# Optimization experiments

Hardware: AMD Instinct MI355X
Metric: run time of the kernel (lower is better)

## Reference

```python
import jax, jax.numpy as jnp
import numpy as np

TH = 0.8  # ratio-test threshold (init kwarg)


def _cdist(d1, d2):
    # Euclidean distance matrix: ||a||^2 + ||b||^2 - 2 a.b, clamped and sqrt'd
    d1_sq = jnp.sum(d1 * d1, axis=1, keepdims=True)          # [B1,1]
    d2_sq = jnp.sum(d2 * d2, axis=1, keepdims=True).T        # [1,B2]
    dm = d1_sq + d2_sq - 2.0 * (d1 @ d2.T)                   # [B1,B2]
    return jnp.sqrt(jnp.clip(dm, 0.0, None))


def setup_inputs() -> dict:
    key = jax.random.key(0)
    k1, k2 = jax.random.split(key)
    desc1 = jax.random.normal(k1, (8192, 512), dtype=jnp.float32)
    desc2 = jax.random.normal(k2, (8192, 512), dtype=jnp.float32)
    return {"desc1": desc1, "desc2": desc2}


def reference(desc1, desc2):
    # match_snn: nearest + second-nearest neighbor, Lowe ratio test.
    # jit-friendly padded form: instead of compacting rows passing the ratio
    # test (data-dependent B3), we return full-size (B1,) arrays plus the
    # boolean validity mask; masked entries have dist 0.
    dm = _cdist(desc1, desc2)                                # [B1,B2]
    neg_vals, idxs = jax.lax.top_k(-dm, 2)                   # two smallest
    vals = -neg_vals                                         # [B1,2]
    ratio = vals[:, 0] / vals[:, 1]                          # [B1]
    mask = ratio <= TH                                       # [B1]
    match_dists = jnp.where(mask, ratio, 0.0).reshape(-1, 1)  # [B1,1]
    idxs_in1 = jnp.arange(desc1.shape[0], dtype=jnp.int32)
    matches_idxs = jnp.stack([idxs_in1, idxs[:, 0]], axis=1)  # [B1,2]
    return match_dists, matches_idxs, mask
```

## Files before the change

kernel.cpp:

```cpp
#include <hip/hip_runtime.h>

#define NROWS 8192
#define DIM   512

typedef __attribute__((ext_vector_type(8))) short short8;
typedef __attribute__((ext_vector_type(4))) float f32x4;

__device__ inline unsigned short f2bf(float x) {
    unsigned u = __float_as_uint(x);
    u += 0x7fffu + ((u >> 16) & 1u);
    return (unsigned short)(u >> 16);
}
__device__ inline float bf2f(unsigned short h) {
    return __uint_as_float(((unsigned)h) << 16);
}

__global__ __launch_bounds__(256) void dm_split(const float* __restrict__ d1,
                                                const float* __restrict__ d2,
                                                unsigned short* __restrict__ Ahi,
                                                unsigned short* __restrict__ Alo,
                                                unsigned short* __restrict__ Bhi,
                                                unsigned short* __restrict__ Blo) {
    const long long t = (long long)blockIdx.x * 256 + threadIdx.x;
    const long long e = t * 8;
    const long long half = (long long)NROWS * DIM;
    const bool second = (e >= half);
    const float* src = second ? d2 : d1;
    unsigned short* hid = second ? Bhi : Ahi;
    unsigned short* lod = second ? Blo : Alo;
    const long long o = second ? e - half : e;
    float4 x0 = *(const float4*)(src + o);
    float4 x1 = *(const float4*)(src + o + 4);
    float xs[8] = {x0.x, x0.y, x0.z, x0.w, x1.x, x1.y, x1.z, x1.w};
    unsigned short hs[8], ls[8];
#pragma unroll
    for (int i = 0; i < 8; ++i) {
        hs[i] = f2bf(xs[i]);
        ls[i] = f2bf(xs[i] - bf2f(hs[i]));
    }
    *(short8*)(hid + o) = *(short8*)hs;
    *(short8*)(lod + o) = *(short8*)ls;
}

__global__ __launch_bounds__(256) void dm_norms2(const float* __restrict__ d2,
                                                 float* __restrict__ n2) {
    const int wave = threadIdx.x >> 6;
    const int lane = threadIdx.x & 63;
    const int r = blockIdx.x * 4 + wave;
    const float* src = d2 + (size_t)r * DIM;
    float4 a = *(const float4*)(src + lane * 4);
    float4 b = *(const float4*)(src + 256 + lane * 4);
    float s = a.x * a.x + a.y * a.y + a.z * a.z + a.w * a.w
            + b.x * b.x + b.y * b.y + b.z * b.z + b.w * b.w;
#pragma unroll
    for (int m = 32; m >= 1; m >>= 1) s += __shfl_xor(s, m);
    if (lane == 0) n2[r] = s;
}

#define NSPLIT 16
#define SLICE (NROWS / NSPLIT)
#define NCT   (SLICE / 128)
#define NKT   48

__global__ __launch_bounds__(256, 2) void dm_match_mfma(
        const unsigned short* __restrict__ Ahi, const unsigned short* __restrict__ Alo,
        const unsigned short* __restrict__ Bhi, const unsigned short* __restrict__ Blo,
        const float* __restrict__ n2, float4* __restrict__ part) {
    __shared__ short8 Bs[8][64];

    const int tid = threadIdx.x;
    const int l   = tid & 63;
    const int w   = tid >> 6;
    const int rb  = blockIdx.x >> 4;
    const int sp  = blockIdx.x & (NSPLIT - 1);
    const int row0 = rb * 128;
    const int col0 = sp * SLICE;
    const int lr = l & 15;
    const int lk = l >> 4;

    const long long arow0 = (long long)(row0 + (2 * w + 0) * 16 + lr) * DIM + lk * 8;
    const long long arow1 = (long long)(row0 + (2 * w + 1) * 16 + lr) * DIM + lk * 8;

    float v0[8], v1[8];
    int   i0[8], i1[8];
#pragma unroll
    for (int s = 0; s < 8; ++s) { v0[s] = 3.0e38f; v1[s] = 3.0e38f; i0[s] = 0; i1[s] = 0; }

    for (int ct = 0; ct < NCT; ++ct) {
        const int colblk = col0 + ct * 128;
        const long long brow0 = (long long)(colblk + (2 * w + 0) * 16 + lr) * DIM + lk * 8;
        const long long brow1 = (long long)(colblk + (2 * w + 1) * 16 + lr) * DIM + lk * 8;

        f32x4 acc[2][8];
#pragma unroll
        for (int m = 0; m < 2; ++m)
#pragma unroll
            for (int n = 0; n < 8; ++n) acc[m][n] = (f32x4){0.f, 0.f, 0.f, 0.f};

        short8 ga0 = *(const short8*)(Ahi + arow0);
        short8 ga1 = *(const short8*)(Ahi + arow1);
        short8 gb0 = *(const short8*)(Bhi + brow0);
        short8 gb1 = *(const short8*)(Bhi + brow1);

        for (int kt = 0; kt < NKT; ++kt) {
            const int kn = (kt + 1 < NKT) ? kt + 1 : kt;
            const int pn = kn >> 4;
            const unsigned short* An = (pn < 2) ? Ahi : Alo;
            const unsigned short* Bn = (pn == 1) ? Blo : Bhi;
            const int k0n = (kn & 15) * 32;
            short8 na0 = *(const short8*)(An + arow0 + k0n);
            short8 na1 = *(const short8*)(An + arow1 + k0n);
            short8 nb0 = *(const short8*)(Bn + brow0 + k0n);
            short8 nb1 = *(const short8*)(Bn + brow1 + k0n);

            __syncthreads();
            Bs[2 * w + 0][l] = gb0;
            Bs[2 * w + 1][l] = gb1;
            __syncthreads();

            short8 b0 = Bs[0][l], b1 = Bs[1][l], b2 = Bs[2][l], b3 = Bs[3][l];
            short8 b4 = Bs[4][l], b5 = Bs[5][l], b6 = Bs[6][l], b7 = Bs[7][l];

            acc[0][0] = __builtin_amdgcn_mfma_f32_16x16x32_bf16(ga0, b0, acc[0][0], 0, 0, 0);
            acc[0][1] = __builtin_amdgcn_mfma_f32_16x16x32_bf16(ga0, b1, acc[0][1], 0, 0, 0);
            acc[0][2] = __builtin_amdgcn_mfma_f32_16x16x32_bf16(ga0, b2, acc[0][2], 0, 0, 0);
            acc[0][3] = __builtin_amdgcn_mfma_f32_16x16x32_bf16(ga0, b3, acc[0][3], 0, 0, 0);
            acc[0][4] = __builtin_amdgcn_mfma_f32_16x16x32_bf16(ga0, b4, acc[0][4], 0, 0, 0);
            acc[0][5] = __builtin_amdgcn_mfma_f32_16x16x32_bf16(ga0, b5, acc[0][5], 0, 0, 0);
            acc[0][6] = __builtin_amdgcn_mfma_f32_16x16x32_bf16(ga0, b6, acc[0][6], 0, 0, 0);
            acc[0][7] = __builtin_amdgcn_mfma_f32_16x16x32_bf16(ga0, b7, acc[0][7], 0, 0, 0);
            acc[1][0] = __builtin_amdgcn_mfma_f32_16x16x32_bf16(ga1, b0, acc[1][0], 0, 0, 0);
            acc[1][1] = __builtin_amdgcn_mfma_f32_16x16x32_bf16(ga1, b1, acc[1][1], 0, 0, 0);
            acc[1][2] = __builtin_amdgcn_mfma_f32_16x16x32_bf16(ga1, b2, acc[1][2], 0, 0, 0);
            acc[1][3] = __builtin_amdgcn_mfma_f32_16x16x32_bf16(ga1, b3, acc[1][3], 0, 0, 0);
            acc[1][4] = __builtin_amdgcn_mfma_f32_16x16x32_bf16(ga1, b4, acc[1][4], 0, 0, 0);
            acc[1][5] = __builtin_amdgcn_mfma_f32_16x16x32_bf16(ga1, b5, acc[1][5], 0, 0, 0);
            acc[1][6] = __builtin_amdgcn_mfma_f32_16x16x32_bf16(ga1, b6, acc[1][6], 0, 0, 0);
            acc[1][7] = __builtin_amdgcn_mfma_f32_16x16x32_bf16(ga1, b7, acc[1][7], 0, 0, 0);

            ga0 = na0; ga1 = na1; gb0 = nb0; gb1 = nb1;
        }

#pragma unroll
        for (int n = 0; n < 8; ++n) {
            const int c = colblk + n * 16 + lr;
            const float nv = n2[c];
#pragma unroll
            for (int m = 0; m < 2; ++m) {
#pragma unroll
                for (int r = 0; r < 4; ++r) {
                    const float s = fmaf(-2.f, acc[m][n][r], nv);
                    const int slot = m * 4 + r;
                    if (s < v1[slot]) {
                        if (s < v0[slot]) { v1[slot] = v0[slot]; i1[slot] = i0[slot];
                                            v0[slot] = s;        i0[slot] = c; }
                        else              { v1[slot] = s;        i1[slot] = c; }
                    }
                }
            }
        }
    }

#pragma unroll
    for (int slot = 0; slot < 8; ++slot) {
        float a0 = v0[slot], a1 = v1[slot];
        int   ai0 = i0[slot], ai1 = i1[slot];
#pragma unroll
        for (int m = 1; m <= 8; m <<= 1) {
            float b0 = __shfl_xor(a0, m);
            float b1 = __shfl_xor(a1, m);
            int   bi0 = __shfl_xor(ai0, m);
            int   bi1 = __shfl_xor(ai1, m);
            if (b0 < a0 || (b0 == a0 && bi0 < ai0)) {
                if (a0 < b1 || (a0 == b1 && ai0 < bi1)) { a1 = a0; ai1 = ai0; }
                else                                    { a1 = b1; ai1 = bi1; }
                a0 = b0; ai0 = bi0;
            } else if (b0 < a1 || (b0 == a1 && bi0 < ai1)) {
                a1 = b0; ai1 = bi0;
            }
        }
        if (lr == 0) {
            const int row = row0 + w * 32 + (slot >> 2) * 16 + lk * 4 + (slot & 3);
            float4 p;
            p.x = a0; p.y = a1;
            p.z = __int_as_float(ai0); p.w = __int_as_float(ai1);
            part[row * NSPLIT + sp] = p;
        }
    }
}

#define NCAND 32
__global__ __launch_bounds__(256) void dm_rescore(const float* __restrict__ d1,
                                                  const float* __restrict__ d2,
                                                  const float4* __restrict__ part,
                                                  float* __restrict__ out) {
    __shared__ double cv[NCAND];
    __shared__ int    cj[NCAND];
    const int row = blockIdx.x;
    const int c = threadIdx.x >> 3;
    const int p = threadIdx.x & 7;
    float4 P = part[row * NSPLIT + (c >> 1)];
    const int j = __float_as_int((c & 1) ? P.w : P.z);

    const float* a = d1 + (size_t)row * DIM + p * 64;
    const float* b = d2 + (size_t)j   * DIM + p * 64;
    double s = 0.0;
#pragma unroll
    for (int q = 0; q < 64; q += 4) {
        float4 x = *(const float4*)(a + q);
        float4 y = *(const float4*)(b + q);
        double e;
        e = (double)x.x - (double)y.x; s = fma(e, e, s);
        e = (double)x.y - (double)y.y; s = fma(e, e, s);
        e = (double)x.z - (double)y.z; s = fma(e, e, s);
        e = (double)x.w - (double)y.w; s = fma(e, e, s);
    }
    s += __shfl_xor(s, 1);
    s += __shfl_xor(s, 2);
    s += __shfl_xor(s, 4);
    if (p == 0) { cv[c] = s; cj[c] = j; }
    __syncthreads();
    if (threadIdx.x == 0) {
        double b0 = 1.0e300, b1 = 1.0e300;
        int    j0 = 0, j1 = 0;
        for (int q = 0; q < NCAND; ++q) {
            const double v = cv[q];
            const int   jj = cj[q];
            if (v < b0 || (v == b0 && jj < j0)) { b1 = b0; j1 = j0; b0 = v; j0 = jj; }
            else if (v < b1 || (v == b1 && jj < j1)) { b1 = v; j1 = jj; }
        }
        const double d0  = sqrt(b0);
        const double d1v = sqrt(b1);
        const double dr  = d0 / d1v;
        const bool mask = (dr <= 0.8);
        out[row] = mask ? (float)dr : 0.f;
        out[NROWS + 2 * row]     = (float)row;
        out[NROWS + 2 * row + 1] = (float)j0;
        out[3 * NROWS + row] = mask ? 1.f : 0.f;
    }
}

__global__ __launch_bounds__(256) void dmfb_norms(const float* __restrict__ d1,
                                                  const float* __restrict__ d2,
                                                  double* __restrict__ n1,
                                                  double* __restrict__ n2) {
    const int wave = threadIdx.x >> 6;
    const int lane = threadIdx.x & 63;
    const int r = blockIdx.x * 4 + wave;
    const float* src = (r < NROWS) ? (d1 + (size_t)r * DIM)
                                   : (d2 + (size_t)(r - NROWS) * DIM);
    float4 a = *(const float4*)(src + lane * 4);
    float4 b = *(const float4*)(src + 256 + lane * 4);
    double s = (double)a.x * a.x + (double)a.y * a.y
             + (double)a.z * a.z + (double)a.w * a.w
             + (double)b.x * b.x + (double)b.y * b.y
             + (double)b.z * b.z + (double)b.w * b.w;
#pragma unroll
    for (int m = 32; m >= 1; m >>= 1) s += __shfl_xor(s, m);
    if (lane == 0) {
        if (r < NROWS) n1[r] = s;
        else           n2[r - NROWS] = s;
    }
}

__global__ __launch_bounds__(256) void dmfb_match(const float* __restrict__ d1,
                                                  const float* __restrict__ d2,
                                                  const double* __restrict__ n2,
                                                  double* __restrict__ pv0,
                                                  double* __restrict__ pv1,
                                                  int* __restrict__ pi0) {
    __shared__ float As[32][64];
    __shared__ float Bsh[32][64];
    const int rb   = blockIdx.x / 4;
    const int sp   = blockIdx.x % 4;
    const int row0 = rb * 64;
    const int col0 = sp * 2048;
    const int tid = threadIdx.x;
    const int tx  = tid & 15;
    const int ty  = tid >> 4;
    const int sc  = tid >> 3;
    const int sk  = (tid & 7) << 2;
    double v0[4], v1[4];
    int    i0[4];
#pragma unroll
    for (int r = 0; r < 4; ++r) { v0[r] = 1.0e300; v1[r] = 1.0e300; i0[r] = 0; }
    for (int ct = 0; ct < 32; ++ct) {
        const int c0 = col0 + ct * 64;
        double acc64[4][4];
#pragma unroll
        for (int r = 0; r < 4; ++r)
#pragma unroll
            for (int c = 0; c < 4; ++c) acc64[r][c] = 0.0;
        for (int kk = 0; kk < DIM; kk += 32) {
            float4 a0 = *(const float4*)(d1 + (size_t)(row0 + sc)      * DIM + kk + sk);
            float4 a1 = *(const float4*)(d1 + (size_t)(row0 + sc + 32) * DIM + kk + sk);
            float4 b0 = *(const float4*)(d2 + (size_t)(c0  + sc)      * DIM + kk + sk);
            float4 b1 = *(const float4*)(d2 + (size_t)(c0  + sc + 32) * DIM + kk + sk);
            __syncthreads();
            {
                const int wc0 = sc ^ sk;
                const int wc1 = (sc + 32) ^ sk;
                As[sk + 0][wc0] = a0.x; As[sk + 1][wc0] = a0.y;
                As[sk + 2][wc0] = a0.z; As[sk + 3][wc0] = a0.w;
                As[sk + 0][wc1] = a1.x; As[sk + 1][wc1] = a1.y;
                As[sk + 2][wc1] = a1.z; As[sk + 3][wc1] = a1.w;
                Bsh[sk + 0][wc0] = b0.x; Bsh[sk + 1][wc0] = b0.y;
                Bsh[sk + 2][wc0] = b0.z; Bsh[sk + 3][wc0] = b0.w;
                Bsh[sk + 0][wc1] = b1.x; Bsh[sk + 1][wc1] = b1.y;
                Bsh[sk + 2][wc1] = b1.z; Bsh[sk + 3][wc1] = b1.w;
            }
            __syncthreads();
            float acc[4][4];
#pragma unroll
            for (int r = 0; r < 4; ++r)
#pragma unroll
                for (int c = 0; c < 4; ++c) acc[r][c] = 0.f;
#pragma unroll
            for (int k = 0; k < 32; ++k) {
                const int rsw = (k >> 2) << 2;
                float4 a = *(const float4*)&As[k][(ty * 4) ^ rsw];
                float4 b = *(const float4*)&Bsh[k][(tx * 4) ^ rsw];
                acc[0][0] = fmaf(a.x, b.x, acc[0][0]);
                acc[0][1] = fmaf(a.x, b.y, acc[0][1]);
                acc[0][2] = fmaf(a.x, b.z, acc[0][2]);
                acc[0][3] = fmaf(a.x, b.w, acc[0][3]);
                acc[1][0] = fmaf(a.y, b.x, acc[1][0]);
                acc[1][1] = fmaf(a.y, b.y, acc[1][1]);
                acc[1][2] = fmaf(a.y, b.z, acc[1][2]);
                acc[1][3] = fmaf(a.y, b.w, acc[1][3]);
                acc[2][0] = fmaf(a.z, b.x, acc[2][0]);
                acc[2][1] = fmaf(a.z, b.y, acc[2][1]);
                acc[2][2] = fmaf(a.z, b.z, acc[2][2]);
                acc[2][3] = fmaf(a.z, b.w, acc[2][3]);
                acc[3][0] = fmaf(a.w, b.x, acc[3][0]);
                acc[3][1] = fmaf(a.w, b.y, acc[3][1]);
                acc[3][2] = fmaf(a.w, b.z, acc[3][2]);
                acc[3][3] = fmaf(a.w, b.w, acc[3][3]);
            }
#pragma unroll
            for (int r = 0; r < 4; ++r)
#pragma unroll
                for (int c = 0; c < 4; ++c) acc64[r][c] += (double)acc[r][c];
        }
        const int cbase = c0 + tx * 4;
        double nna[4];
#pragma unroll
        for (int c = 0; c < 4; ++c) nna[c] = n2[cbase + c];
#pragma unroll
        for (int r = 0; r < 4; ++r) {
#pragma unroll
            for (int c = 0; c < 4; ++c) {
                const double s = nna[c] - 2.0 * acc64[r][c];
                const int j = cbase + c;
                if (s < v0[r]) { v1[r] = v0[r]; v0[r] = s; i0[r] = j; }
                else if (s < v1[r]) { v1[r] = s; }
            }
        }
    }
#pragma unroll
    for (int r = 0; r < 4; ++r) {
        double a0 = v0[r], a1 = v1[r];
        int    ai = i0[r];
#pragma unroll
        for (int m = 1; m <= 8; m <<= 1) {
            double b0 = __shfl_xor(a0, m);
            double b1 = __shfl_xor(a1, m);
            int    bi = __shfl_xor(ai, m);
            bool take = (b0 < a0) || (b0 == a0 && bi < ai);
            if (take) { a1 = fmin(a0, b1); a0 = b0; ai = bi; }
            else      { a1 = fmin(a1, b0); }
        }
        if (tx == 0) {
            const int row = row0 + ty * 4 + r;
            pv0[sp * NROWS + row] = a0;
            pv1[sp * NROWS + row] = a1;
            pi0[sp * NROWS + row] = ai;
        }
    }
}

__global__ __launch_bounds__(256) void dmfb_finalize(const double* __restrict__ n1,
                                                     const double* __restrict__ pv0,
                                                     const double* __restrict__ pv1,
                                                     const int* __restrict__ pi0,
                                                     float* __restrict__ out) {
    const int i = blockIdx.x * blockDim.x + threadIdx.x;
    if (i >= NROWS) return;
    double a0 = pv0[i], a1 = pv1[i];
    int    ai = pi0[i];
#pragma unroll
    for (int h = 1; h < 4; ++h) {
        const double b0 = pv0[h * NROWS + i];
        const double b1 = pv1[h * NROWS + i];
        const int    bi = pi0[h * NROWS + i];
        bool take = (b0 < a0) || (b0 == a0 && bi < ai);
        if (take) { a1 = fmin(a0, b1); a0 = b0; ai = bi; }
        else      { a1 = fmin(a1, b0); }
    }
    const double nn = n1[i];
    const double d0  = sqrt(fmax(nn + a0, 0.0));
    const double d1v = sqrt(fmax(nn + a1, 0.0));
    const float ratio = (float)(d0 / d1v);
    const bool mask = (ratio <= 0.8f);
    out[i] = mask ? ratio : 0.f;
    out[NROWS + 2 * i]     = (float)i;
    out[NROWS + 2 * i + 1] = (float)ai;
    out[3 * NROWS + i] = mask ? 1.f : 0.f;
}

extern "C" void kernel_launch(void* const* d_in, const int* in_sizes, int n_in,
                              void* d_out, int out_size, void* d_ws, size_t ws_size,
                              hipStream_t stream) {
    const float* d1 = (const float*)d_in[0];
    const float* d2 = (const float*)d_in[1];
    float* out = (float*)d_out;

    const size_t ELEMS = (size_t)NROWS * DIM;
    const size_t need = 4 * ELEMS * 2 + NROWS * 4
                      + (size_t)NROWS * NSPLIT * 16;
    if (ws_size >= need) {
        unsigned short* Ahi = (unsigned short*)d_ws;
        unsigned short* Alo = Ahi + ELEMS;
        unsigned short* Bhi = Alo + ELEMS;
        unsigned short* Blo = Bhi + ELEMS;
        float* n2 = (float*)(Blo + ELEMS);
        float4* part = (float4*)(n2 + NROWS);

        dm_split<<<(2 * ELEMS) / (256 * 8), 256, 0, stream>>>(d1, d2, Ahi, Alo, Bhi, Blo);
        dm_norms2<<<NROWS / 4, 256, 0, stream>>>(d2, n2);
        dm_match_mfma<<<(NROWS / 128) * NSPLIT, 256, 0, stream>>>(Ahi, Alo, Bhi, Blo, n2, part);
        dm_rescore<<<NROWS, 256, 0, stream>>>(d1, d2, part, out);
    } else {
        double* n1  = (double*)d_ws;
        double* n2  = n1 + NROWS;
        double* pv0 = n2 + NROWS;
        double* pv1 = pv0 + 4 * NROWS;
        int*    pi0 = (int*)(pv1 + 4 * NROWS);
        dmfb_norms<<<(2 * NROWS) / 4, 256, 0, stream>>>(d1, d2, n1, n2);
        dmfb_match<<<(NROWS / 64) * 4, 256, 0, stream>>>(d1, d2, n2, pv0, pv1, pi0);
        dmfb_finalize<<<NROWS / 256, 256, 0, stream>>>(n1, pv0, pv1, pi0, out);
    }
}
```

Measured before the change: 594.9 us.

## Stream B tiles into LDS via async global_load_lds with triple buffering

Replaces the register-staged B tile (global load to register, then LDS store between two barriers) with direct global-to-LDS DMA loads into a three-deep ring buffer, issued two steps ahead. The ct and kt loops are flattened into one pipelined loop so prefetch continues across column tiles, and the epilogue runs when a tile's K steps finish. The intent is to drop the extra LDS write and one barrier per step and to hide global latency behind the MFMAs. It relies on a hand-written vmcnt wait count and a single barrier per step, so correctness depends on in-order completion and on the buffer reuse distance being large enough.

```diff
diff --git a/kernel.cpp b/kernel.cpp
--- a/kernel.cpp
+++ b/kernel.cpp
@@ -61,12 +61,18 @@
 #define SLICE (NROWS / NSPLIT)
 #define NCT   (SLICE / 128)
 #define NKT   48
+#define NSTEPS (NCT * NKT)
+
+__device__ __forceinline__ void gload_lds16(const void* g, void* l) {
+    __builtin_amdgcn_global_load_lds((const unsigned int*)g, (unsigned int*)l,
+                                     16, 0, 0);
+}
 
 __global__ __launch_bounds__(256, 2) void dm_match_mfma(
         const unsigned short* __restrict__ Ahi, const unsigned short* __restrict__ Alo,
         const unsigned short* __restrict__ Bhi, const unsigned short* __restrict__ Blo,
         const float* __restrict__ n2, float4* __restrict__ part) {
-    __shared__ short8 Bs[8][64];
+    __shared__ short8 Bs[3][8][64];
 
     const int tid = threadIdx.x;
     const int l   = tid & 63;
@@ -80,84 +86,99 @@
 
     const long long arow0 = (long long)(row0 + (2 * w + 0) * 16 + lr) * DIM + lk * 8;
     const long long arow1 = (long long)(row0 + (2 * w + 1) * 16 + lr) * DIM + lk * 8;
+    const long long brow0 = (long long)((2 * w + 0) * 16 + lr) * DIM + lk * 8;
+    const long long brow1 = (long long)((2 * w + 1) * 16 + lr) * DIM + lk * 8;
+
+    auto loadA = [&](int step, short8& a0, short8& a1) {
+        const int kt = step % NKT;
+        const unsigned short* A = (kt < 32) ? Ahi : Alo;
+        const int k0 = (kt & 15) * 32;
+        a0 = *(const short8*)(A + arow0 + k0);
+        a1 = *(const short8*)(A + arow1 + k0);
+    };
+    auto issueDMA = [&](int step) {
+        const int ct = step / NKT;
+        const int kt = step % NKT;
+        const unsigned short* B = (kt >= 16 && kt < 32) ? Blo : Bhi;
+        const long long cb = (long long)(col0 + ct * 128) * DIM + (kt & 15) * 32;
+        const int buf = step % 3;
+        gload_lds16(B + cb + brow0, &Bs[buf][2 * w + 0][0]);
+        gload_lds16(B + cb + brow1, &Bs[buf][2 * w + 1][0]);
+    };
 
     float v0[8], v1[8];
     int   i0[8], i1[8];
 #pragma unroll
     for (int s = 0; s < 8; ++s) { v0[s] = 3.0e38f; v1[s] = 3.0e38f; i0[s] = 0; i1[s] = 0; }
 
-    for (int ct = 0; ct < NCT; ++ct) {
-        const int colblk = col0 + ct * 128;
-        const long long brow0 = (long long)(colblk + (2 * w + 0) * 16 + lr) * DIM + lk * 8;
-        const long long brow1 = (long long)(colblk + (2 * w + 1) * 16 + lr) * DIM + lk * 8;
-
-        f32x4 acc[2][8];
-#pragma unroll
-        for (int m = 0; m < 2; ++m)
-#pragma unroll
-            for (int n = 0; n < 8; ++n) acc[m][n] = (f32x4){0.f, 0.f, 0.f, 0.f};
-
-        short8 ga0 = *(const short8*)(Ahi + arow0);
-        short8 ga1 = *(const short8*)(Ahi + arow1);
-        short8 gb0 = *(const short8*)(Bhi + brow0);
-        short8 gb1 = *(const short8*)(Bhi + brow1);
-
-        for (int kt = 0; kt < NKT; ++kt) {
-            const int kn = (kt + 1 < NKT) ? kt + 1 : kt;
-            const int pn = kn >> 4;
-            const unsigned short* An = (pn < 2) ? Ahi : Alo;
-            const unsigned short* Bn = (pn == 1) ? Blo : Bhi;
-            const int k0n = (kn & 15) * 32;
-            short8 na0 = *(const short8*)(An + arow0 + k0n);
-            short8 na1 = *(const short8*)(An + arow1 + k0n);
-            short8 nb0 = *(const short8*)(Bn + brow0 + k0n);
-            short8 nb1 = *(const short8*)(Bn + brow1 + k0n);
-
-            __syncthreads();
-            Bs[2 * w + 0][l] = gb0;
-            Bs[2 * w + 1][l] = gb1;
-            __syncthreads();
-
-            short8 b0 = Bs[0][l], b1 = Bs[1][l], b2 = Bs[2][l], b3 = Bs[3][l];
-            short8 b4 = Bs[4][l], b5 = Bs[5][l], b6 = Bs[6][l], b7 = Bs[7][l];
-
-            acc[0][0] = __builtin_amdgcn_mfma_f32_16x16x32_bf16(ga0, b0, acc[0][0], 0, 0, 0);
-            acc[0][1] = __builtin_amdgcn_mfma_f32_16x16x32_bf16(ga0, b1, acc[0][1], 0, 0, 0);
-            acc[0][2] = __builtin_amdgcn_mfma_f32_16x16x32_bf16(ga0, b2, acc[0][2], 0, 0, 0);
-            acc[0][3] = __builtin_amdgcn_mfma_f32_16x16x32_bf16(ga0, b3, acc[0][3], 0, 0, 0);
-            acc[0][4] = __builtin_amdgcn_mfma_f32_16x16x32_bf16(ga0, b4, acc[0][4], 0, 0, 0);
-            acc[0][5] = __builtin_amdgcn_mfma_f32_16x16x32_bf16(ga0, b5, acc[0][5], 0, 0, 0);
-            acc[0][6] = __builtin_amdgcn_mfma_f32_16x16x32_bf16(ga0, b6, acc[0][6], 0, 0, 0);
-            acc[0][7] = __builtin_amdgcn_mfma_f32_16x16x32_bf16(ga0, b7, acc[0][7], 0, 0, 0);
-            acc[1][0] = __builtin_amdgcn_mfma_f32_16x16x32_bf16(ga1, b0, acc[1][0], 0, 0, 0);
-            acc[1][1] = __builtin_amdgcn_mfma_f32_16x16x32_bf16(ga1, b1, acc[1][1], 0, 0, 0);
-            acc[1][2] = __builtin_amdgcn_mfma_f32_16x16x32_bf16(ga1, b2, acc[1][2], 0, 0, 0);
-            acc[1][3] = __builtin_amdgcn_mfma_f32_16x16x32_bf16(ga1, b3, acc[1][3], 0, 0, 0);
-            acc[1][4] = __builtin_amdgcn_mfma_f32_16x16x32_bf16(ga1, b4, acc[1][4], 0, 0, 0);
-            acc[1][5] = __builtin_amdgcn_mfma_f32_16x16x32_bf16(ga1, b5, acc[1][5], 0, 0, 0);
-            acc[1][6] = __builtin_amdgcn_mfma_f32_16x16x32_bf16(ga1, b6, acc[1][6], 0, 0, 0);
-            acc[1][7] = __builtin_amdgcn_mfma_f32_16x16x32_bf16(ga1, b7, acc[1][7], 0, 0, 0);
-
-            ga0 = na0; ga1 = na1; gb0 = nb0; gb1 = nb1;
-        }
-
-#pragma unroll
-        for (int n = 0; n < 8; ++n) {
-            const int c = colblk + n * 16 + lr;
-            const float nv = n2[c];
-#pragma unroll
-            for (int m = 0; m < 2; ++m) {
-#pragma unroll
-                for (int r = 0; r < 4; ++r) {
-                    const float s = fmaf(-2.f, acc[m][n][r], nv);
-                    const int slot = m * 4 + r;
-                    if (s < v1[slot]) {
-                        if (s < v0[slot]) { v1[slot] = v0[slot]; i1[slot] = i0[slot];
-                                            v0[slot] = s;        i0[slot] = c; }
-                        else              { v1[slot] = s;        i1[slot] = c; }
+    f32x4 acc[2][8];
+#pragma unroll
+    for (int m = 0; m < 2; ++m)
+#pragma unroll
+        for (int n = 0; n < 8; ++n) acc[m][n] = (f32x4){0.f, 0.f, 0.f, 0.f};
+
+    short8 cA0, cA1, nA0, nA1;
+    loadA(0, cA0, cA1);
+    issueDMA(0);
+    issueDMA(1);
+
+    for (int s = 0; s < NSTEPS; ++s) {
+        loadA((s + 1 < NSTEPS) ? s + 1 : s, nA0, nA1);
+        asm volatile("s_waitcnt vmcnt(4)" ::: "memory");
+        __builtin_amdgcn_s_barrier();
+        __builtin_amdgcn_sched_barrier(0);
+
+        const int buf = s % 3;
+        short8 b0 = Bs[buf][0][l], b1 = Bs[buf][1][l];
+        short8 b2 = Bs[buf][2][l], b3 = Bs[buf][3][l];
+        short8 b4 = Bs[buf][4][l], b5 = Bs[buf][5][l];
+        short8 b6 = Bs[buf][6][l], b7 = Bs[buf][7][l];
+
+        if (s + 2 < NSTEPS) issueDMA(s + 2);
+
+        acc[0][0] = __builtin_amdgcn_mfma_f32_16x16x32_bf16(cA0, b0, acc[0][0], 0, 0, 0);
+        acc[0][1] = __builtin_amdgcn_mfma_f32_16x16x32_bf16(cA0, b1, acc[0][1], 0, 0, 0);
+        acc[0][2] = __builtin_amdgcn_mfma_f32_16x16x32_bf16(cA0, b2, acc[0][2], 0, 0, 0);
+        acc[0][3] = __builtin_amdgcn_mfma_f32_16x16x32_bf16(cA0, b3, acc[0][3], 0, 0, 0);
+        acc[0][4] = __builtin_amdgcn_mfma_f32_16x16x32_bf16(cA0, b4, acc[0][4], 0, 0, 0);
+        acc[0][5] = __builtin_amdgcn_mfma_f32_16x16x32_bf16(cA0, b5, acc[0][5], 0, 0, 0);
+        acc[0][6] = __builtin_amdgcn_mfma_f32_16x16x32_bf16(cA0, b6, acc[0][6], 0, 0, 0);
+        acc[0][7] = __builtin_amdgcn_mfma_f32_16x16x32_bf16(cA0, b7, acc[0][7], 0, 0, 0);
+        acc[1][0] = __builtin_amdgcn_mfma_f32_16x16x32_bf16(cA1, b0, acc[1][0], 0, 0, 0);
+        acc[1][1] = __builtin_amdgcn_mfma_f32_16x16x32_bf16(cA1, b1, acc[1][1], 0, 0, 0);
+        acc[1][2] = __builtin_amdgcn_mfma_f32_16x16x32_bf16(cA1, b2, acc[1][2], 0, 0, 0);
+        acc[1][3] = __builtin_amdgcn_mfma_f32_16x16x32_bf16(cA1, b3, acc[1][3], 0, 0, 0);
+        acc[1][4] = __builtin_amdgcn_mfma_f32_16x16x32_bf16(cA1, b4, acc[1][4], 0, 0, 0);
+        acc[1][5] = __builtin_amdgcn_mfma_f32_16x16x32_bf16(cA1, b5, acc[1][5], 0, 0, 0);
+        acc[1][6] = __builtin_amdgcn_mfma_f32_16x16x32_bf16(cA1, b6, acc[1][6], 0, 0, 0);
+        acc[1][7] = __builtin_amdgcn_mfma_f32_16x16x32_bf16(cA1, b7, acc[1][7], 0, 0, 0);
+
+        cA0 = nA0; cA1 = nA1;
+
+        if (s % NKT == NKT - 1) {
+            const int colblk = col0 + (s / NKT) * 128;
+#pragma unroll
+            for (int n = 0; n < 8; ++n) {
+                const int c = colblk + n * 16 + lr;
+                const float nv = n2[c];
+#pragma unroll
+                for (int m = 0; m < 2; ++m) {
+#pragma unroll
+                    for (int r = 0; r < 4; ++r) {
+                        const float sv = fmaf(-2.f, acc[m][n][r], nv);
+                        const int slot = m * 4 + r;
+                        if (sv < v1[slot]) {
+                            if (sv < v0[slot]) { v1[slot] = v0[slot]; i1[slot] = i0[slot];
+                                                 v0[slot] = sv;       i0[slot] = c; }
+                            else               { v1[slot] = sv;       i1[slot] = c; }
+                        }
                     }
                 }
             }
+#pragma unroll
+            for (int m = 0; m < 2; ++m)
+#pragma unroll
+                for (int n = 0; n < 8; ++n) acc[m][n] = (f32x4){0.f, 0.f, 0.f, 0.f};
         }
     }
 
```

Result: slower. 614.0 us (+3.2%).

## Double row tile per block and reduce top-2 across lanes per column tile

Applied to the files above, without the earlier changes.

Each block now covers 256 rows instead of 128, with four 16-row A fragments per wave against the shared B tile, so every B load and LDS broadcast is reused across twice as many MFMAs. The per-slot top-2 registers are replaced by a per-column-tile shuffle reduction whose merged result is held by one designated lane per row, which frees registers for the larger accumulator array. The grid shrinks to 512 blocks. The trade-off is more accumulator registers (128 floats) with launch bounds still requesting 2 blocks per SIMD, a shuffle reduction after every column tile instead of once at the end, and possibly lower occupancy or register spills.

```diff
diff --git a/kernel.cpp b/kernel.cpp
--- a/kernel.cpp
+++ b/kernel.cpp
@@ -73,45 +73,46 @@
     const int w   = tid >> 6;
     const int rb  = blockIdx.x >> 4;
     const int sp  = blockIdx.x & (NSPLIT - 1);
-    const int row0 = rb * 128;
+    const int row0 = rb * 256;
     const int col0 = sp * SLICE;
     const int lr = l & 15;
     const int lk = l >> 4;
 
-    const long long arow0 = (long long)(row0 + (2 * w + 0) * 16 + lr) * DIM + lk * 8;
-    const long long arow1 = (long long)(row0 + (2 * w + 1) * 16 + lr) * DIM + lk * 8;
-
-    float v0[8], v1[8];
-    int   i0[8], i1[8];
-#pragma unroll
-    for (int s = 0; s < 8; ++s) { v0[s] = 3.0e38f; v1[s] = 3.0e38f; i0[s] = 0; i1[s] = 0; }
+    long long arow[4];
+#pragma unroll
+    for (int m = 0; m < 4; ++m)
+        arow[m] = (long long)(row0 + w * 64 + m * 16 + lr) * DIM + lk * 8;
+    const long long brow0 = (long long)((2 * w + 0) * 16 + lr) * DIM + lk * 8;
+    const long long brow1 = (long long)((2 * w + 1) * 16 + lr) * DIM + lk * 8;
+
+    float rv0 = 3.0e38f, rv1 = 3.0e38f;
+    int   ri0 = 0, ri1 = 0;
 
     for (int ct = 0; ct < NCT; ++ct) {
         const int colblk = col0 + ct * 128;
-        const long long brow0 = (long long)(colblk + (2 * w + 0) * 16 + lr) * DIM + lk * 8;
-        const long long brow1 = (long long)(colblk + (2 * w + 1) * 16 + lr) * DIM + lk * 8;
-
-        f32x4 acc[2][8];
-#pragma unroll
-        for (int m = 0; m < 2; ++m)
+        const long long bbase = (long long)colblk * DIM;
+
+        f32x4 acc[4][8];
+#pragma unroll
+        for (int m = 0; m < 4; ++m)
 #pragma unroll
             for (int n = 0; n < 8; ++n) acc[m][n] = (f32x4){0.f, 0.f, 0.f, 0.f};
 
-        short8 ga0 = *(const short8*)(Ahi + arow0);
-        short8 ga1 = *(const short8*)(Ahi + arow1);
-        short8 gb0 = *(const short8*)(Bhi + brow0);
-        short8 gb1 = *(const short8*)(Bhi + brow1);
+        short8 ga[4], na[4];
+#pragma unroll
+        for (int m = 0; m < 4; ++m) ga[m] = *(const short8*)(Ahi + arow[m]);
+        short8 gb0 = *(const short8*)(Bhi + bbase + brow0);
+        short8 gb1 = *(const short8*)(Bhi + bbase + brow1);
 
         for (int kt = 0; kt < NKT; ++kt) {
             const int kn = (kt + 1 < NKT) ? kt + 1 : kt;
-            const int pn = kn >> 4;
-            const unsigned short* An = (pn < 2) ? Ahi : Alo;
-            const unsigned short* Bn = (pn == 1) ? Blo : Bhi;
+            const unsigned short* An = (kn < 32) ? Ahi : Alo;
+            const unsigned short* Bn = (kn >= 16 && kn < 32) ? Blo : Bhi;
             const int k0n = (kn & 15) * 32;
-            short8 na0 = *(const short8*)(An + arow0 + k0n);
-            short8 na1 = *(const short8*)(An + arow1 + k0n);
-            short8 nb0 = *(const short8*)(Bn + brow0 + k0n);
-            short8 nb1 = *(const short8*)(Bn + brow1 + k0n);
+#pragma unroll
+            for (int m = 0; m < 4; ++m) na[m] = *(const short8*)(An + arow[m] + k0n);
+            short8 nb0 = *(const short8*)(Bn + bbase + brow0 + k0n);
+            short8 nb1 = *(const short8*)(Bn + bbase + brow1 + k0n);
 
             __syncthreads();
             Bs[2 * w + 0][l] = gb0;
@@ -121,71 +122,73 @@
             short8 b0 = Bs[0][l], b1 = Bs[1][l], b2 = Bs[2][l], b3 = Bs[3][l];
             short8 b4 = Bs[4][l], b5 = Bs[5][l], b6 = Bs[6][l], b7 = Bs[7][l];
 
-            acc[0][0] = __builtin_amdgcn_mfma_f32_16x16x32_bf16(ga0, b0, acc[0][0], 0, 0, 0);
-            acc[0][1] = __builtin_amdgcn_mfma_f32_16x16x32_bf16(ga0, b1, acc[0][1], 0, 0, 0);
-            acc[0][2] = __builtin_amdgcn_mfma_f32_16x16x32_bf16(ga0, b2, acc[0][2], 0, 0, 0);
-            acc[0][3] = __builtin_amdgcn_mfma_f32_16x16x32_bf16(ga0, b3, acc[0][3], 0, 0, 0);
-            acc[0][4] = __builtin_amdgcn_mfma_f32_16x16x32_bf16(ga0, b4, acc[0][4], 0, 0, 0);
-            acc[0][5] = __builtin_amdgcn_mfma_f32_16x16x32_bf16(ga0, b5, acc[0][5], 0, 0, 0);
-            acc[0][6] = __builtin_amdgcn_mfma_f32_16x16x32_bf16(ga0, b6, acc[0][6], 0, 0, 0);
-            acc[0][7] = __builtin_amdgcn_mfma_f32_16x16x32_bf16(ga0, b7, acc[0][7], 0, 0, 0);
-            acc[1][0] = __builtin_amdgcn_mfma_f32_16x16x32_bf16(ga1, b0, acc[1][0], 0, 0, 0);
-            acc[1][1] = __builtin_amdgcn_mfma_f32_16x16x32_bf16(ga1, b1, acc[1][1], 0, 0, 0);
-            acc[1][2] = __builtin_amdgcn_mfma_f32_16x16x32_bf16(ga1, b2, acc[1][2], 0, 0, 0);
-            acc[1][3] = __builtin_amdgcn_mfma_f32_16x16x32_bf16(ga1, b3, acc[1][3], 0, 0, 0);
-            acc[1][4] = __builtin_amdgcn_mfma_f32_16x16x32_bf16(ga1, b4, acc[1][4], 0, 0, 0);
-            acc[1][5] = __builtin_amdgcn_mfma_f32_16x16x32_bf16(ga1, b5, acc[1][5], 0, 0, 0);
-            acc[1][6] = __builtin_amdgcn_mfma_f32_16x16x32_bf16(ga1, b6, acc[1][6], 0, 0, 0);
-            acc[1][7] = __builtin_amdgcn_mfma_f32_16x16x32_bf16(ga1, b7, acc[1][7], 0, 0, 0);
-
-            ga0 = na0; ga1 = na1; gb0 = nb0; gb1 = nb1;
-        }
-
-#pragma unroll
-        for (int n = 0; n < 8; ++n) {
-            const int c = colblk + n * 16 + lr;
-            const float nv = n2[c];
-#pragma unroll
-            for (int m = 0; m < 2; ++m) {
-#pragma unroll
-                for (int r = 0; r < 4; ++r) {
-                    const float s = fmaf(-2.f, acc[m][n][r], nv);
-                    const int slot = m * 4 + r;
-                    if (s < v1[slot]) {
-                        if (s < v0[slot]) { v1[slot] = v0[slot]; i1[slot] = i0[slot];
-                                            v0[slot] = s;        i0[slot] = c; }
-                        else              { v1[slot] = s;        i1[slot] = c; }
+#pragma unroll
+            for (int m = 0; m < 4; ++m) {
+                acc[m][0] = __builtin_amdgcn_mfma_f32_16x16x32_bf16(ga[m], b0, acc[m][0], 0, 0, 0);
+                acc[m][1] = __builtin_amdgcn_mfma_f32_16x16x32_bf16(ga[m], b1, acc[m][1], 0, 0, 0);
+                acc[m][2] = __builtin_amdgcn_mfma_f32_16x16x32_bf16(ga[m], b2, acc[m][2], 0, 0, 0);
+                acc[m][3] = __builtin_amdgcn_mfma_f32_16x16x32_bf16(ga[m], b3, acc[m][3], 0, 0, 0);
+                acc[m][4] = __builtin_amdgcn_mfma_f32_16x16x32_bf16(ga[m], b4, acc[m][4], 0, 0, 0);
+                acc[m][5] = __builtin_amdgcn_mfma_f32_16x16x32_bf16(ga[m], b5, acc[m][5], 0, 0, 0);
+                acc[m][6] = __builtin_amdgcn_mfma_f32_16x16x32_bf16(ga[m], b6, acc[m][6], 0, 0, 0);
+                acc[m][7] = __builtin_amdgcn_mfma_f32_16x16x32_bf16(ga[m], b7, acc[m][7], 0, 0, 0);
+            }
+#pragma unroll
+            for (int m = 0; m < 4; ++m) ga[m] = na[m];
+            gb0 = nb0; gb1 = nb1;
+        }
+
+        float n2v[8];
+#pragma unroll
+        for (int n = 0; n < 8; ++n) n2v[n] = n2[colblk + n * 16 + lr];
+
+#pragma unroll
+        for (int m = 0; m < 4; ++m) {
+#pragma unroll
+            for (int r = 0; r < 4; ++r) {
+                float a0 = 3.0e38f, a1 = 3.0e38f;
+                int   ai0 = 0, ai1 = 0;
+#pragma unroll
+                for (int n = 0; n < 8; ++n) {
+                    const float sv = fmaf(-2.f, acc[m][n][r], n2v[n]);
+                    const int c = colblk + n * 16 + lr;
+                    if (sv < a1) {
+                        if (sv < a0) { a1 = a0; ai1 = ai0; a0 = sv; ai0 = c; }
+                        else         { a1 = sv; ai1 = c; }
                     }
                 }
+#pragma unroll
+                for (int msk = 1; msk <= 8; msk <<= 1) {
+                    float b0 = __shfl_xor(a0, msk);
+                    float b1 = __shfl_xor(a1, msk);
+                    int   bi0 = __shfl_xor(ai0, msk);
+                    int   bi1 = __shfl_xor(ai1, msk);
+                    if (b0 < a0 || (b0 == a0 && bi0 < ai0)) {
+                        if (a0 < b1 || (a0 == b1 && ai0 < bi1)) { a1 = a0; ai1 = ai0; }
+                        else                                    { a1 = b1; ai1 = bi1; }
+                        a0 = b0; ai0 = bi0;
+                    } else if (b0 < a1 || (b0 == a1 && bi0 < ai1)) {
+                        a1 = b0; ai1 = bi0;
+                    }
+                }
+                const bool mine = (lr == (m * 4 + r));
+                const bool cfirst = (a0 < rv0);
+                float n0 = cfirst ? a0 : rv0;
+                int   ni0 = cfirst ? ai0 : ri0;
+                float n1; int ni1;
+                if (cfirst) { const bool rs = (rv0 <= a1); n1 = rs ? rv0 : a1; ni1 = rs ? ri0 : ai1; }
+                else        { const bool rs = (rv1 <= a0); n1 = rs ? rv1 : a0; ni1 = rs ? ri1 : ai0; }
+                if (mine) { rv0 = n0; ri0 = ni0; rv1 = n1; ri1 = ni1; }
             }
         }
     }
 
-#pragma unroll
-    for (int slot = 0; slot < 8; ++slot) {
-        float a0 = v0[slot], a1 = v1[slot];
-        int   ai0 = i0[slot], ai1 = i1[slot];
-#pragma unroll
-        for (int m = 1; m <= 8; m <<= 1) {
-            float b0 = __shfl_xor(a0, m);
-            float b1 = __shfl_xor(a1, m);
-            int   bi0 = __shfl_xor(ai0, m);
-            int   bi1 = __shfl_xor(ai1, m);
-            if (b0 < a0 || (b0 == a0 && bi0 < ai0)) {
-                if (a0 < b1 || (a0 == b1 && ai0 < bi1)) { a1 = a0; ai1 = ai0; }
-                else                                    { a1 = b1; ai1 = bi1; }
-                a0 = b0; ai0 = bi0;
-            } else if (b0 < a1 || (b0 == a1 && bi0 < ai1)) {
-                a1 = b0; ai1 = bi0;
-            }
-        }
-        if (lr == 0) {
-            const int row = row0 + w * 32 + (slot >> 2) * 16 + lk * 4 + (slot & 3);
-            float4 p;
-            p.x = a0; p.y = a1;
-            p.z = __int_as_float(ai0); p.w = __int_as_float(ai1);
-            part[row * NSPLIT + sp] = p;
-        }
+    {
+        const int row = row0 + w * 64 + (lr >> 2) * 16 + lk * 4 + (lr & 3);
+        float4 p;
+        p.x = rv0; p.y = rv1;
+        p.z = __int_as_float(ri0); p.w = __int_as_float(ri1);
+        part[row * NSPLIT + sp] = p;
     }
 }
 
@@ -428,7 +431,7 @@
 
         dm_split<<<(2 * ELEMS) / (256 * 8), 256, 0, stream>>>(d1, d2, Ahi, Alo, Bhi, Blo);
         dm_norms2<<<NROWS / 4, 256, 0, stream>>>(d2, n2);
-        dm_match_mfma<<<(NROWS / 128) * NSPLIT, 256, 0, stream>>>(Ahi, Alo, Bhi, Blo, n2, part);
+        dm_match_mfma<<<(NROWS / 256) * NSPLIT, 256, 0, stream>>>(Ahi, Alo, Bhi, Blo, n2, part);
         dm_rescore<<<NROWS, 256, 0, stream>>>(d1, d2, part, out);
     } else {
         double* n1  = (double*)d_ws;
```

Result: faster. 510.4 us (-14.2%).
